# Kernel tuning notes

Hardware: AMD Instinct MI355X
Metric: run time of the kernel (lower is better)

## Reference

```python
import jax, jax.numpy as jnp
import numpy as np

B, T, H = 256, 512, 1024


def setup_inputs() -> dict:
    key = jax.random.key(0)
    ks = jax.random.split(key, 11)
    s = 1.0 / np.sqrt(H)
    u = lambda k, shape: jax.random.uniform(k, shape, jnp.float32, -s, s)
    return {
        "x": jax.random.normal(ks[0], (B, T), jnp.float32),
        "W_ih1": u(ks[1], (4 * H, 1)),
        "W_hh1": u(ks[2], (4 * H, H)),
        "b_ih1": u(ks[3], (4 * H,)),
        "b_hh1": u(ks[4], (4 * H,)),
        "W_ih2": u(ks[5], (4 * H, H)),
        "W_hh2": u(ks[6], (4 * H, H)),
        "b_ih2": u(ks[7], (4 * H,)),
        "b_hh2": u(ks[8], (4 * H,)),
        "W_out": u(ks[9], (1, H)),
        "b_out": u(ks[10], (1,)),
        "future": 0,
    }


def _lstm_cell(x, h, c, W_ih, W_hh, b):
    # PyTorch LSTMCell gate order: i, f, g, o
    gates = x @ W_ih.T + h @ W_hh.T + b
    i, f, g, o = jnp.split(gates, 4, axis=-1)
    c_new = jax.nn.sigmoid(f) * c + jax.nn.sigmoid(i) * jnp.tanh(g)
    h_new = jax.nn.sigmoid(o) * jnp.tanh(c_new)
    return h_new, c_new


def reference(x, W_ih1, W_hh1, b_ih1, b_hh1, W_ih2, W_hh2, b_ih2, b_hh2, W_out, b_out, future):
    Bn = x.shape[0]
    Hd = W_hh1.shape[1]
    b1 = b_ih1 + b_hh1
    b2 = b_ih2 + b_hh2

    def step(carry, x_t):
        h1, c1, h2, c2 = carry
        h1, c1 = _lstm_cell(x_t, h1, c1, W_ih1, W_hh1, b1)
        h2, c2 = _lstm_cell(h1, h2, c2, W_ih2, W_hh2, b2)
        out = h2 @ W_out.T + b_out  # [B, 1]
        return (h1, c1, h2, c2), out

    xs = x.T[:, :, None]  # [T, B, 1]
    carry0 = tuple(jnp.zeros((Bn, Hd), x.dtype) for _ in range(4))
    carry, outs = jax.lax.scan(step, carry0, xs)  # outs: [T, B, 1]
    outputs = [outs[:, :, 0].T]  # [B, T]

    # closed-loop future prediction (future is a static Python int)
    out = outs[-1]
    for _ in range(future):
        carry, out = step(carry, out)
        outputs.append(out)
    return jnp.concatenate(outputs, axis=1)
```

## Files before the change

kernel.cpp:

```cpp
#include <hip/hip_runtime.h>
#include <hip/hip_cooperative_groups.h>
#include <math.h>

namespace cg = cooperative_groups;

#define Bsz 256
#define Tsz 512
#define GSTR 258

using half8 = __attribute__((ext_vector_type(8))) _Float16;
using half4 = __attribute__((ext_vector_type(4))) _Float16;
using f32x4 = __attribute__((ext_vector_type(4))) float;

#define MFMA_V(acc, a, b) (acc) = __builtin_amdgcn_mfma_f32_16x16x32_f16((a), (b), (acc), 0, 0, 0)
#define INV2048 (1.0f / 2048.0f)

__device__ __forceinline__ float sigm(float v)   { return 1.0f / (1.0f + expf(-v)); }
__device__ __forceinline__ float tanh_f(float v) { float e = expf(2.0f * v); return 1.0f - 2.0f / (e + 1.0f); }

__device__ __forceinline__ void split8(const float* p, half8& hi, half8& lo) {
    float4 v0 = *(const float4*)p, v1 = *(const float4*)(p + 4);
    float vv[8] = {v0.x, v0.y, v0.z, v0.w, v1.x, v1.y, v1.z, v1.w};
    #pragma unroll
    for (int j = 0; j < 8; ++j) {
        hi[j] = (_Float16)vv[j];
        lo[j] = (_Float16)((vv[j] - (float)hi[j]) * 2048.0f);
    }
}

__device__ __forceinline__ void st_h4(_Float16* p, half4 v) {
    unsigned long long u;
    __builtin_memcpy(&u, &v, 8);
    __hip_atomic_store((unsigned long long*)(void*)p, u,
                       __ATOMIC_RELAXED, __HIP_MEMORY_SCOPE_AGENT);
}
__device__ __forceinline__ void st_f(float* p, float v) {
    __hip_atomic_store(p, v, __ATOMIC_RELAXED, __HIP_MEMORY_SCOPE_AGENT);
}

__device__ __forceinline__ void step_barrier(unsigned* bar0, unsigned* bar1,
                                             unsigned* phase2, unsigned* dummyv,
                                             int bx, int isLead, unsigned xcc,
                                             unsigned nLead, unsigned it1) {
    __syncthreads();
    if (threadIdx.x == 0) {
        unsigned old = __hip_atomic_fetch_add(&bar0[(bx & 15) << 5], 1u,
                                              __ATOMIC_RELAXED, __HIP_MEMORY_SCOPE_AGENT);
        if ((old & 15u) == 15u)
            __hip_atomic_fetch_add(bar1, 1u, __ATOMIC_RELAXED, __HIP_MEMORY_SCOPE_AGENT);
        const bool l2i = (it1 & 3u) == 0u;
        if (l2i) {
            if (isLead) {
                while (__hip_atomic_load(bar1, __ATOMIC_RELAXED, __HIP_MEMORY_SCOPE_AGENT) < 16u * it1)
                    __builtin_amdgcn_s_sleep(1);
                __hip_atomic_fetch_add(&dummyv[xcc << 5], 1u,
                                       __ATOMIC_ACQ_REL, __HIP_MEMORY_SCOPE_AGENT);
                __hip_atomic_fetch_add(phase2, 1u,
                                       __ATOMIC_RELAXED, __HIP_MEMORY_SCOPE_AGENT);
            }
            while (__hip_atomic_load(phase2, __ATOMIC_RELAXED, __HIP_MEMORY_SCOPE_AGENT) < nLead * (it1 >> 2))
                __builtin_amdgcn_s_sleep(1);
        } else {
            while (__hip_atomic_load(bar1, __ATOMIC_RELAXED, __HIP_MEMORY_SCOPE_AGENT) < 16u * it1)
                __builtin_amdgcn_s_sleep(1);
        }
        asm volatile("buffer_inv sc0" ::: "memory");
    }
    __syncthreads();
}

__global__ __launch_bounds__(512, 1) void lstm_persist(
    const float* __restrict__ x,
    const float* __restrict__ W_ih1, const float* __restrict__ W_hh1,
    const float* __restrict__ b_ih1, const float* __restrict__ b_hh1,
    const float* __restrict__ W_ih2, const float* __restrict__ W_hh2,
    const float* __restrict__ b_ih2, const float* __restrict__ b_hh2,
    const float* __restrict__ W_out, const float* __restrict__ b_out,
    float* __restrict__ out, char* __restrict__ ws)
{
    __shared__ float gAcc[32 * GSTR];
    __shared__ float poArr[2 * GSTR];
    __shared__ float bp[32], wihp[32], woutp[8];
    __shared__ float bouts_s;
    __shared__ unsigned isLead_s, xcc_s, nLead_s;

    cg::grid_group grid = cg::this_grid();

    const int tid  = threadIdx.x;
    const int lane = tid & 63;
    const int wv   = tid >> 6;
    const int m    = lane & 15;
    const int quad = lane >> 4;
    const int bx   = blockIdx.x;
    const bool isL2 = (bx >= 128);
    const int rg   = isL2 ? (bx - 128) : bx;
    const int HO   = rg << 3;

    float*    xT       = (float*)ws;
    _Float16* hswz     = (_Float16*)(ws + (512 << 10));
    float*    partials = (float*)(ws + (512 << 10) + (8 << 20));
    unsigned* bar0     = (unsigned*)(ws + (512 << 10) + (8 << 20) + (512 << 10));
    unsigned* bar1     = bar0 + 1024;
    unsigned* phase2   = bar0 + 1056;
    unsigned* nLeadCt  = bar0 + 1057;
    unsigned* claimA   = bar0 + 1088;
    unsigned* dummyv   = bar0 + 1536;

    #define HBUF(p, l, hl) (hswz + ((((p) << 2) | ((l) << 1) | (hl)) << 18))

    if (bx == 0)
        for (int i = tid; i < 2048; i += 512) bar0[i] = 0u;
    if (tid < 32) {
        const int row = ((tid & 3) << 10) + HO + (tid >> 2);
        if (!isL2) {
            bp[tid]   = b_ih1[row] + b_hh1[row];
            wihp[tid] = W_ih1[row];
        } else {
            bp[tid] = b_ih2[row] + b_hh2[row];
            if (tid < 8) woutp[tid] = W_out[HO + tid];
        }
        if (tid == 0) bouts_s = b_out[0];
    }
    {
        const int gidx = bx * 512 + tid;
        *(float4*)((char*)hswz + (6u << 20) + (size_t)gidx * 16) = make_float4(0, 0, 0, 0);
        xT[gidx] = x[(gidx & 255) * Tsz + (gidx >> 8)];
    }

    grid.sync();

    if (tid == 0) {
        unsigned xcc;
        asm volatile("s_getreg_b32 %0, hwreg(HW_REG_XCC_ID)" : "=s"(xcc));
        xcc &= 7u;
        xcc_s = xcc;
        unsigned old = __hip_atomic_fetch_add(&claimA[xcc << 5], 1u,
                                              __ATOMIC_RELAXED, __HIP_MEMORY_SCOPE_AGENT);
        isLead_s = (old == 0u);
        if (old == 0u)
            __hip_atomic_fetch_add(nLeadCt, 1u,
                                   __ATOMIC_RELAXED, __HIP_MEMORY_SCOPE_AGENT);
    }
    grid.sync();
    if (tid == 0)
        nLead_s = __hip_atomic_load(nLeadCt, __ATOMIC_RELAXED, __HIP_MEMORY_SCOPE_AGENT);
    __syncthreads();
    const int      isLead = (int)isLead_s;
    const unsigned xcc    = xcc_s;
    const unsigned nLead  = nLead_s;

    const int b_ep = tid & 255, hg = tid >> 8;
    const int k0e  = HO + (hg << 2);
    const int wofs = ((b_ep >> 4) << 14) + ((k0e >> 5) << 9)
                   + (((b_ep & 15) | (((k0e >> 3) & 3) << 4)) << 3) + (k0e & 7);

    if (!isL2) {
        half8 wh[2][4], wl[2][4];
        #pragma unroll
        for (int mt = 0; mt < 2; ++mt) {
            const int pr = (mt << 4) + m;
            const size_t rw = (size_t)(((pr & 3) << 10) + HO + (pr >> 2)) << 10;
            #pragma unroll
            for (int kt = 0; kt < 4; ++kt) {
                const int k = (wv << 7) + (kt << 5) + (quad << 3);
                split8(W_hh1 + rw + k, wh[mt][kt], wl[mt][kt]);
            }
        }
        for (int idx = tid; idx < 8192; idx += 512) {
            const int p = idx >> 8, b = idx & 255;
            gAcc[p * GSTR + b] = bp[p] + xT[b] * wihp[p];
        }
        __syncthreads();
        float cr[4] = {0, 0, 0, 0};

        for (int it = 0; it <= Tsz; ++it) {
            const int sW = it & 3;
            const int sR = (it + 3) & 3;
            const int sP = it & 3;

            float xnext = 0.0f;
            if (it + 1 < Tsz) xnext = xT[((it + 1) << 8) + b_ep];

            if (wv == 0 && it >= 2) {
                const float* pp = partials + (sP << 15) + (bx << 7);
                float s = pp[lane] + pp[lane + 64];
                s += __shfl_xor(s, 32); s += __shfl_xor(s, 16); s += __shfl_xor(s, 8);
                s += __shfl_xor(s, 4);  s += __shfl_xor(s, 2);  s += __shfl_xor(s, 1);
                if (lane == 0) st_f(&out[(bx << 9) + (it - 2)], bouts_s + s);
            }

            if (it < Tsz) {
                const _Float16* bhB = HBUF(sR, 0, 0);
                const _Float16* blB = HBUF(sR, 0, 1);
                const int lo_off = (wv << 11) + (lane << 3);
                #pragma unroll 2
                for (int bi = 0; bi < 16; ++bi) {
                    const int btl = (bi + (wv << 1)) & 15;
                    const _Float16* ph = bhB + (btl << 14) + lo_off;
                    const _Float16* pl = blB + (btl << 14) + lo_off;
                    half8 bh[4], bl[4];
                    #pragma unroll
                    for (int kt = 0; kt < 4; ++kt) {
                        bh[kt] = *(const half8*)(ph + (kt << 9));
                        bl[kt] = *(const half8*)(pl + (kt << 9));
                    }
                    f32x4 a0[2] = {(f32x4){0,0,0,0}, (f32x4){0,0,0,0}};
                    f32x4 a1[2] = {(f32x4){0,0,0,0}, (f32x4){0,0,0,0}};
                    #pragma unroll
                    for (int kt = 0; kt < 4; ++kt) {
                        MFMA_V(a0[0], wh[0][kt], bh[kt]);
                        MFMA_V(a1[0], wh[0][kt], bl[kt]);
                        MFMA_V(a1[0], wl[0][kt], bh[kt]);
                        MFMA_V(a0[1], wh[1][kt], bh[kt]);
                        MFMA_V(a1[1], wh[1][kt], bl[kt]);
                        MFMA_V(a1[1], wl[1][kt], bh[kt]);
                    }
                    const int col = (btl << 4) + m;
                    #pragma unroll
                    for (int mt = 0; mt < 2; ++mt)
                        #pragma unroll
                        for (int r = 0; r < 4; ++r)
                            atomicAdd(&gAcc[((mt << 4) + (quad << 2) + r) * GSTR + col],
                                      a0[mt][r] + a1[mt][r] * INV2048);
                }
            }

            __syncthreads();

            if (it < Tsz) {
                half4 hhi, hlo;
                #pragma unroll
                for (int j = 0; j < 4; ++j) {
                    const int p = (hg << 4) + (j << 2);
                    const float gi = gAcc[(p + 0) * GSTR + b_ep];
                    const float gf = gAcc[(p + 1) * GSTR + b_ep];
                    const float gg = gAcc[(p + 2) * GSTR + b_ep];
                    const float go = gAcc[(p + 3) * GSTR + b_ep];
                    const float c  = sigm(gf) * cr[j] + sigm(gi) * tanh_f(gg);
                    cr[j] = c;
                    const float hn = sigm(go) * tanh_f(c);
                    hhi[j] = (_Float16)hn;
                    hlo[j] = (_Float16)((hn - (float)hhi[j]) * 2048.0f);
                }
                st_h4(HBUF(sW, 0, 0) + wofs, hhi);
                st_h4(HBUF(sW, 0, 1) + wofs, hlo);
                if (it + 1 < Tsz) {
                    #pragma unroll
                    for (int p = (hg << 4); p < (hg << 4) + 16; ++p)
                        gAcc[p * GSTR + b_ep] = bp[p] + xnext * wihp[p];
                }
            }

            step_barrier(bar0, bar1, phase2, dummyv, bx, isLead, xcc, nLead,
                         (unsigned)(it + 1));
        }
    } else {
        half8 wh[2][8], wl[2][8];
        #pragma unroll
        for (int mt = 0; mt < 2; ++mt) {
            const int pr = (mt << 4) + m;
            const size_t rw = (size_t)(((pr & 3) << 10) + HO + (pr >> 2)) << 10;
            #pragma unroll
            for (int kt = 0; kt < 8; ++kt) {
                const int k = (wv << 8) + (kt << 5) + (quad << 3);
                const float* p = (k < 1024) ? (W_ih2 + rw + k)
                                            : (W_hh2 + rw + k - 1024);
                split8(p, wh[mt][kt], wl[mt][kt]);
            }
        }
        for (int idx = tid; idx < 8192; idx += 512) {
            const int p = idx >> 8, b = idx & 255;
            gAcc[p * GSTR + b] = bp[p];
        }
        __syncthreads();
        float cr[4] = {0, 0, 0, 0};

        for (int it = 0; it <= Tsz; ++it) {
            const int sR1 = (it + 3) & 3;
            const int sW2 = (it + 3) & 3;
            const int sR2 = (it + 2) & 3;
            const int sP  = it & 3;
            const int sPW = (it + 1) & 3;

            if (wv == 0 && it >= 2) {
                const float* pp = partials + (sP << 15) + (bx << 7);
                float s = pp[lane] + pp[lane + 64];
                s += __shfl_xor(s, 32); s += __shfl_xor(s, 16); s += __shfl_xor(s, 8);
                s += __shfl_xor(s, 4);  s += __shfl_xor(s, 2);  s += __shfl_xor(s, 1);
                if (lane == 0) st_f(&out[(bx << 9) + (it - 2)], bouts_s + s);
            }

            if (it >= 1) {
                const bool hi2 = (wv >= 4);
                const _Float16* bhB = hi2 ? HBUF(sR2, 1, 0) : HBUF(sR1, 0, 0);
                const _Float16* blB = hi2 ? HBUF(sR2, 1, 1) : HBUF(sR1, 0, 1);
                const int lo_off = ((wv & 3) << 12) + (lane << 3);
                #pragma unroll 1
                for (int bi = 0; bi < 16; ++bi) {
                    const int btl = (bi + (wv << 1)) & 15;
                    const _Float16* ph = bhB + (btl << 14) + lo_off;
                    const _Float16* pl = blB + (btl << 14) + lo_off;
                    half8 bh[8], bl[8];
                    #pragma unroll
                    for (int kt = 0; kt < 8; ++kt) {
                        bh[kt] = *(const half8*)(ph + (kt << 9));
                        bl[kt] = *(const half8*)(pl + (kt << 9));
                    }
                    f32x4 a0[2] = {(f32x4){0,0,0,0}, (f32x4){0,0,0,0}};
                    f32x4 a1[2] = {(f32x4){0,0,0,0}, (f32x4){0,0,0,0}};
                    #pragma unroll
                    for (int kt = 0; kt < 8; ++kt) {
                        MFMA_V(a0[0], wh[0][kt], bh[kt]);
                        MFMA_V(a1[0], wh[0][kt], bl[kt]);
                        MFMA_V(a1[0], wl[0][kt], bh[kt]);
                        MFMA_V(a0[1], wh[1][kt], bh[kt]);
                        MFMA_V(a1[1], wh[1][kt], bl[kt]);
                        MFMA_V(a1[1], wl[1][kt], bh[kt]);
                    }
                    const int col = (btl << 4) + m;
                    #pragma unroll
                    for (int mt = 0; mt < 2; ++mt)
                        #pragma unroll
                        for (int r = 0; r < 4; ++r)
                            atomicAdd(&gAcc[((mt << 4) + (quad << 2) + r) * GSTR + col],
                                      a0[mt][r] + a1[mt][r] * INV2048);
                }
            }

            __syncthreads();

            if (it >= 1) {
                half4 hhi, hlo;
                float po = 0.0f;
                #pragma unroll
                for (int j = 0; j < 4; ++j) {
                    const int p = (hg << 4) + (j << 2);
                    const float gi = gAcc[(p + 0) * GSTR + b_ep];
                    const float gf = gAcc[(p + 1) * GSTR + b_ep];
                    const float gg = gAcc[(p + 2) * GSTR + b_ep];
                    const float go = gAcc[(p + 3) * GSTR + b_ep];
                    const float c  = sigm(gf) * cr[j] + sigm(gi) * tanh_f(gg);
                    cr[j] = c;
                    const float hn = sigm(go) * tanh_f(c);
                    hhi[j] = (_Float16)hn;
                    hlo[j] = (_Float16)((hn - (float)hhi[j]) * 2048.0f);
                    po += hn * woutp[(hg << 2) + j];
                }
                st_h4(HBUF(sW2, 1, 0) + wofs, hhi);
                st_h4(HBUF(sW2, 1, 1) + wofs, hlo);
                poArr[hg * GSTR + b_ep] = po;
                #pragma unroll
                for (int p = (hg << 4); p < (hg << 4) + 16; ++p)
                    gAcc[p * GSTR + b_ep] = bp[p];
            }
            __syncthreads();
            if (it >= 1 && tid < 256) {
                const float s = poArr[tid] + poArr[GSTR + tid];
                st_f(&partials[(sPW << 15) + (tid << 7) + rg], s);
            }

            step_barrier(bar0, bar1, phase2, dummyv, bx, isLead, xcc, nLead,
                         (unsigned)(it + 1));
        }
    }

    if (wv == 0) {
        const float* pp = partials + (1 << 15) + (bx << 7);
        float s = pp[lane] + pp[lane + 64];
        s += __shfl_xor(s, 32); s += __shfl_xor(s, 16); s += __shfl_xor(s, 8);
        s += __shfl_xor(s, 4);  s += __shfl_xor(s, 2);  s += __shfl_xor(s, 1);
        if (lane == 0) st_f(&out[(bx << 9) + (Tsz - 1)], bouts_s + s);
    }
    #undef HBUF
}

extern "C" void kernel_launch(void* const* d_in, const int* in_sizes, int n_in,
                              void* d_out, int out_size, void* d_ws, size_t ws_size,
                              hipStream_t stream)
{
    const float* x     = (const float*)d_in[0];
    const float* W_ih1 = (const float*)d_in[1];
    const float* W_hh1 = (const float*)d_in[2];
    const float* b_ih1 = (const float*)d_in[3];
    const float* b_hh1 = (const float*)d_in[4];
    const float* W_ih2 = (const float*)d_in[5];
    const float* W_hh2 = (const float*)d_in[6];
    const float* b_ih2 = (const float*)d_in[7];
    const float* b_hh2 = (const float*)d_in[8];
    const float* W_out = (const float*)d_in[9];
    const float* b_out = (const float*)d_in[10];
    float* out = (float*)d_out;
    char*  ws  = (char*)d_ws;

    void* args[] = {
        (void*)&x,
        (void*)&W_ih1, (void*)&W_hh1, (void*)&b_ih1, (void*)&b_hh1,
        (void*)&W_ih2, (void*)&W_hh2, (void*)&b_ih2, (void*)&b_hh2,
        (void*)&W_out, (void*)&b_out, (void*)&out, (void*)&ws,
    };
    hipLaunchCooperativeKernel((const void*)lstm_persist,
                               dim3(256), dim3(512), args, 0, stream);
}
```

Before: 46.28 ms.

## Replace flat grid barrier with hierarchical per-XCC leader barrier

The per-step grid barrier becomes two levels. Blocks arrive on a counter for their XCC, one leader per XCC waits for all its local blocks and then meets the other leaders on a global counter, and each leader releases its XCC's blocks through a per-XCC flag. Before, every block polled a single global counter that all blocks incremented through 16 strided sub-counters. The aim is to cut cross-XCC atomic traffic and polling contention, at the cost of an extra serial hop through the leaders.

```diff
diff --git a/kernel.cpp b/kernel.cpp
--- a/kernel.cpp
+++ b/kernel.cpp
@@ -38,31 +38,34 @@
     __hip_atomic_store(p, v, __ATOMIC_RELAXED, __HIP_MEMORY_SCOPE_AGENT);
 }
 
-__device__ __forceinline__ void step_barrier(unsigned* bar0, unsigned* bar1,
-                                             unsigned* phase2, unsigned* dummyv,
-                                             int bx, int isLead, unsigned xcc,
-                                             unsigned nLead, unsigned it1) {
+__device__ __forceinline__ unsigned ag_add(unsigned* p, unsigned v) {
+    return __hip_atomic_fetch_add(p, v, __ATOMIC_RELAXED, __HIP_MEMORY_SCOPE_AGENT);
+}
+__device__ __forceinline__ unsigned ag_ld(unsigned* p) {
+    return __hip_atomic_load(p, __ATOMIC_RELAXED, __HIP_MEMORY_SCOPE_AGENT);
+}
+
+__device__ __forceinline__ void step_barrier(unsigned* arrX, unsigned* flagX,
+                                             unsigned* bar1, unsigned* dummyv,
+                                             int isLead, unsigned xcc,
+                                             unsigned nLead, unsigned nBlkX,
+                                             unsigned it1) {
     __syncthreads();
     if (threadIdx.x == 0) {
-        unsigned old = __hip_atomic_fetch_add(&bar0[(bx & 15) << 5], 1u,
-                                              __ATOMIC_RELAXED, __HIP_MEMORY_SCOPE_AGENT);
-        if ((old & 15u) == 15u)
-            __hip_atomic_fetch_add(bar1, 1u, __ATOMIC_RELAXED, __HIP_MEMORY_SCOPE_AGENT);
-        const bool l2i = (it1 & 3u) == 0u;
-        if (l2i) {
-            if (isLead) {
-                while (__hip_atomic_load(bar1, __ATOMIC_RELAXED, __HIP_MEMORY_SCOPE_AGENT) < 16u * it1)
-                    __builtin_amdgcn_s_sleep(1);
+        ag_add(&arrX[xcc << 5], 1u);
+        if (isLead) {
+            while (ag_ld(&arrX[xcc << 5]) < nBlkX * it1)
+                __builtin_amdgcn_s_sleep(1);
+            ag_add(bar1, 1u);
+            while (ag_ld(bar1) < nLead * it1)
+                __builtin_amdgcn_s_sleep(1);
+            if ((it1 & 3u) == 0u)
                 __hip_atomic_fetch_add(&dummyv[xcc << 5], 1u,
                                        __ATOMIC_ACQ_REL, __HIP_MEMORY_SCOPE_AGENT);
-                __hip_atomic_fetch_add(phase2, 1u,
-                                       __ATOMIC_RELAXED, __HIP_MEMORY_SCOPE_AGENT);
-            }
-            while (__hip_atomic_load(phase2, __ATOMIC_RELAXED, __HIP_MEMORY_SCOPE_AGENT) < nLead * (it1 >> 2))
-                __builtin_amdgcn_s_sleep(1);
+            ag_add(&flagX[xcc << 5], 1u);
         } else {
-            while (__hip_atomic_load(bar1, __ATOMIC_RELAXED, __HIP_MEMORY_SCOPE_AGENT) < 16u * it1)
-                __builtin_amdgcn_s_sleep(1);
+            while (ag_ld(&flagX[xcc << 5]) < it1)
+                __builtin_amdgcn_s_sleep(4);
         }
         asm volatile("buffer_inv sc0" ::: "memory");
     }
@@ -82,7 +85,7 @@
     __shared__ float poArr[2 * GSTR];
     __shared__ float bp[32], wihp[32], woutp[8];
     __shared__ float bouts_s;
-    __shared__ unsigned isLead_s, xcc_s, nLead_s;
+    __shared__ unsigned isLead_s, xcc_s, nLead_s, nBlkX_s;
 
     cg::grid_group grid = cg::this_grid();
 
@@ -100,8 +103,9 @@
     _Float16* hswz     = (_Float16*)(ws + (512 << 10));
     float*    partials = (float*)(ws + (512 << 10) + (8 << 20));
     unsigned* bar0     = (unsigned*)(ws + (512 << 10) + (8 << 20) + (512 << 10));
+    unsigned* arrX     = bar0 + 512;
+    unsigned* flagX    = bar0 + 768;
     unsigned* bar1     = bar0 + 1024;
-    unsigned* phase2   = bar0 + 1056;
     unsigned* nLeadCt  = bar0 + 1057;
     unsigned* claimA   = bar0 + 1088;
     unsigned* dummyv   = bar0 + 1536;
@@ -134,20 +138,21 @@
         asm volatile("s_getreg_b32 %0, hwreg(HW_REG_XCC_ID)" : "=s"(xcc));
         xcc &= 7u;
         xcc_s = xcc;
-        unsigned old = __hip_atomic_fetch_add(&claimA[xcc << 5], 1u,
-                                              __ATOMIC_RELAXED, __HIP_MEMORY_SCOPE_AGENT);
+        unsigned old = ag_add(&claimA[xcc << 5], 1u);
         isLead_s = (old == 0u);
         if (old == 0u)
-            __hip_atomic_fetch_add(nLeadCt, 1u,
-                                   __ATOMIC_RELAXED, __HIP_MEMORY_SCOPE_AGENT);
+            ag_add(nLeadCt, 1u);
     }
     grid.sync();
-    if (tid == 0)
-        nLead_s = __hip_atomic_load(nLeadCt, __ATOMIC_RELAXED, __HIP_MEMORY_SCOPE_AGENT);
+    if (tid == 0) {
+        nLead_s = ag_ld(nLeadCt);
+        nBlkX_s = ag_ld(&claimA[xcc_s << 5]);
+    }
     __syncthreads();
     const int      isLead = (int)isLead_s;
     const unsigned xcc    = xcc_s;
     const unsigned nLead  = nLead_s;
+    const unsigned nBlkX  = nBlkX_s;
 
     const int b_ep = tid & 255, hg = tid >> 8;
     const int k0e  = HO + (hg << 2);
@@ -251,7 +256,7 @@
                 }
             }
 
-            step_barrier(bar0, bar1, phase2, dummyv, bx, isLead, xcc, nLead,
+            step_barrier(arrX, flagX, bar1, dummyv, isLead, xcc, nLead, nBlkX,
                          (unsigned)(it + 1));
         }
     } else {
@@ -359,7 +364,7 @@
                 st_f(&partials[(sPW << 15) + (tid << 7) + rg], s);
             }
 
-            step_barrier(bar0, bar1, phase2, dummyv, bx, isLead, xcc, nLead,
+            step_barrier(arrX, flagX, bar1, dummyv, isLead, xcc, nLead, nBlkX,
                          (unsigned)(it + 1));
         }
     }
```

Result: no change. 45.88 ms (-0.9%).
